# Kernel optimization log

Hardware: AMD Instinct MI355X
Metric: run time of the kernel (lower is better)

The kernel has to match this reference:

```python
import jax, jax.numpy as jnp
import numpy as np

N_NODES = 100000
N_EDGES = 1600000
N_FEAT = 128
HIDDEN = 128
N_CLASSES = 8
N_GRAPHS = 256


def setup_inputs() -> dict:
    key = jax.random.key(0)
    ks = jax.random.split(key, 10)
    x = jax.random.normal(ks[0], (N_NODES, N_FEAT), dtype=jnp.float32)
    edge_index = jax.random.randint(ks[1], (2, N_EDGES), 0, N_NODES, dtype=jnp.int64)
    batch = jnp.sort(jax.random.randint(ks[2], (N_NODES,), 0, N_GRAPHS, dtype=jnp.int64))
    s = 1.0 / np.sqrt(HIDDEN)
    W1 = jax.random.normal(ks[3], (N_FEAT, HIDDEN), dtype=jnp.float32) * s
    b1 = jnp.zeros((HIDDEN,), dtype=jnp.float32)
    W2 = jax.random.normal(ks[4], (HIDDEN, HIDDEN), dtype=jnp.float32) * s
    b2 = jnp.zeros((HIDDEN,), dtype=jnp.float32)
    W3 = jax.random.normal(ks[5], (HIDDEN, HIDDEN), dtype=jnp.float32) * s
    b3 = jnp.zeros((HIDDEN,), dtype=jnp.float32)
    Wc1 = jax.random.normal(ks[6], (HIDDEN, HIDDEN // 2), dtype=jnp.float32) * s
    bc1 = jnp.zeros((HIDDEN // 2,), dtype=jnp.float32)
    Wc2 = jax.random.normal(ks[7], (HIDDEN // 2, N_CLASSES), dtype=jnp.float32) * (1.0 / np.sqrt(HIDDEN // 2))
    bc2 = jnp.zeros((N_CLASSES,), dtype=jnp.float32)
    return dict(x=x, edge_index=edge_index, batch=batch, W1=W1, b1=b1,
                W2=W2, b2=b2, W3=W3, b3=b3, Wc1=Wc1, bc1=bc1, Wc2=Wc2, bc2=bc2)


def _gcn_conv(x, W, b, src, dst, dinv_src_dst, deg_inv):
    # PyG GCNConv: h = X W; out = sum_{j->i} norm_ij * h_j + deg_i^{-1} * h_i + b
    h = x @ W  # [N, H]
    msg = h[src] * dinv_src_dst[:, None]            # gather + scale  [E, H]
    agg = jax.ops.segment_sum(msg, dst, num_segments=N_NODES)
    agg = agg + h * deg_inv[:, None]                # self-loop term
    return agg + b


def reference(x, edge_index, batch, W1, b1, W2, b2, W3, b3, Wc1, bc1, Wc2, bc2):
    src, dst = edge_index[0], edge_index[1]
    # symmetric normalization with self-loops: deg_i = 1 + in-degree
    ones = jnp.ones((N_EDGES,), dtype=x.dtype)
    deg = jax.ops.segment_sum(ones, dst, num_segments=N_NODES) + 1.0
    dinv = jax.lax.rsqrt(deg)                        # deg^{-1/2}
    dinv_src_dst = dinv[src] * dinv[dst]             # norm per edge
    deg_inv = 1.0 / deg                              # self-loop norm

    h = jax.nn.relu(_gcn_conv(x, W1, b1, src, dst, dinv_src_dst, deg_inv))
    h = jax.nn.relu(_gcn_conv(h, W2, b2, src, dst, dinv_src_dst, deg_inv))
    h = jax.nn.relu(_gcn_conv(h, W3, b3, src, dst, dinv_src_dst, deg_inv))

    # global_mean_pool over batch ids
    sums = jax.ops.segment_sum(h, batch, num_segments=N_GRAPHS)
    counts = jax.ops.segment_sum(jnp.ones((N_NODES,), dtype=h.dtype), batch,
                                 num_segments=N_GRAPHS)
    pooled = sums / jnp.maximum(counts, 1.0)[:, None]  # [G, H]

    # classifier MLP (eval mode: dropout = identity)
    z = jax.nn.relu(pooled @ Wc1 + bc1)
    return z @ Wc2 + bc2
```

## Files before the change

### kernel.cpp

```cpp
#include <hip/hip_runtime.h>
#include <hip/hip_bf16.h>

#define N_NODES 100000
#define N_EDGES 1600000
#define NFEAT   128
#define HID     128
#define NG      256
#define NCLS    8

typedef __attribute__((ext_vector_type(8))) short bf16x8;
typedef __attribute__((ext_vector_type(4))) float f32x4;

__device__ __forceinline__ unsigned short f2bf(float f) {
    unsigned u = __float_as_uint(f);
    unsigned r = (u + 0x7fffu + ((u >> 16) & 1u)) >> 16;
    return (unsigned short)r;
}


__global__ void zero_int_kernel(int* __restrict__ p, int n) {
    int i = blockIdx.x * 256 + threadIdx.x;
    if (i < n) p[i] = 0;
}

__global__ void count_deg_kernel(const int* __restrict__ dst, int* __restrict__ deg, int e) {
    int i = blockIdx.x * 256 + threadIdx.x;
    if (i < e) atomicAdd(&deg[dst[i]], 1);
}

__global__ void scan1_kernel(const int* __restrict__ deg, int* __restrict__ tmp,
                             int* __restrict__ bsums, int n) {
    __shared__ int s[256];
    int t = threadIdx.x;
    int i = blockIdx.x * 256 + t;
    int v = (i < n) ? deg[i] : 0;
    s[t] = v;
    __syncthreads();
    for (int o = 1; o < 256; o <<= 1) {
        int a = (t >= o) ? s[t - o] : 0;
        __syncthreads();
        s[t] += a;
        __syncthreads();
    }
    if (i < n) tmp[i] = s[t];
    if (t == 255) bsums[blockIdx.x] = s[t];
}

__global__ void scan2_kernel(int* __restrict__ bsums, int nb) {
    __shared__ int s[512];
    int t = threadIdx.x;
    int v = (t < nb) ? bsums[t] : 0;
    s[t] = v;
    __syncthreads();
    for (int o = 1; o < 512; o <<= 1) {
        int a = (t >= o) ? s[t - o] : 0;
        __syncthreads();
        s[t] += a;
        __syncthreads();
    }
    if (t < nb) bsums[t] = s[t] - v;
}

__global__ void scan3_kernel(const int* __restrict__ tmp, const int* __restrict__ bsums,
                             const int* __restrict__ deg, int* __restrict__ row_ptr,
                             int* __restrict__ cursor, float* __restrict__ dinv,
                             float* __restrict__ deg_inv, int n) {
    int b = blockIdx.x;
    int i = b * 256 + threadIdx.x;
    if (i < n) {
        int g  = tmp[i] + bsums[b];
        int d  = deg[i];
        int rp = g - d;
        row_ptr[i] = rp;
        cursor[i]  = rp;
        float df = (float)d + 1.0f;
        dinv[i]    = rsqrtf(df);
        deg_inv[i] = 1.0f / df;
        if (i == n - 1) row_ptr[n] = g;
    }
}

__global__ void fill_edges_kernel(const int* __restrict__ src, const int* __restrict__ dst,
                                  const float* __restrict__ dinv, int* __restrict__ cursor,
                                  uint2* __restrict__ ed, int e) {
    int i = blockIdx.x * 256 + threadIdx.x;
    if (i < e) {
        int s = src[i], d = dst[i];
        int pos = atomicAdd(&cursor[d], 1);
        ed[pos] = make_uint2((unsigned)s, __float_as_uint(dinv[s] * dinv[d]));
    }
}

__global__ void cast_w_kernel(const float* __restrict__ W1, const float* __restrict__ W2,
                              const float* __restrict__ W3,
                              unsigned short* __restrict__ T1, unsigned short* __restrict__ T2,
                              unsigned short* __restrict__ T3) {
    int b = blockIdx.x;
    const float*    W = (b < 64) ? W1 : ((b < 128) ? W2 : W3);
    unsigned short* T = (b < 64) ? T1 : ((b < 128) ? T2 : T3);
    int i = (b & 63) * 256 + threadIdx.x;
    int k = i >> 7, n = i & 127;
    T[n * 128 + k] = f2bf(W[i]);
}

__global__ __launch_bounds__(256) void gemm_mfma_kernel(
        const float* __restrict__ in, unsigned short* __restrict__ H,
        const unsigned short* __restrict__ Wt) {
    const int tid  = threadIdx.x;
    const int wave = tid >> 6;
    const int lane = tid & 63;
    const int r16  = lane & 15;
    const int g    = lane >> 4;
    const int arow = blockIdx.x * 64 + wave * 16 + r16;
    const int arowc = (arow < N_NODES) ? arow : (N_NODES - 1);

    bf16x8 a[4];
#pragma unroll
    for (int kk = 0; kk < 4; ++kk) {
        const float* p = &in[(size_t)arowc * 128 + kk * 32 + g * 8];
        float4 lo = *(const float4*)p;
        float4 hi = *(const float4*)(p + 4);
        union { bf16x8 v; unsigned short u[8]; } t;
        t.u[0] = f2bf(lo.x); t.u[1] = f2bf(lo.y); t.u[2] = f2bf(lo.z); t.u[3] = f2bf(lo.w);
        t.u[4] = f2bf(hi.x); t.u[5] = f2bf(hi.y); t.u[6] = f2bf(hi.z); t.u[7] = f2bf(hi.w);
        a[kk] = t.v;
    }

    const bf16x8* Wv = (const bf16x8*)Wt;
    const int orow0 = blockIdx.x * 64 + wave * 16 + g * 4;

#pragma unroll
    for (int ct = 0; ct < 8; ++ct) {
        const int nb = (ct * 16 + r16) * 16 + g;
        f32x4 acc = {0.f, 0.f, 0.f, 0.f};
#pragma unroll
        for (int kk = 0; kk < 4; ++kk)
            acc = __builtin_amdgcn_mfma_f32_16x16x32_bf16(a[kk], Wv[nb + kk * 4], acc, 0, 0, 0);
        const int col = ct * 16 + r16;
#pragma unroll
        for (int i = 0; i < 4; ++i) {
            int gr = orow0 + i;
            if (gr < N_NODES) H[(size_t)gr * 128 + col] = f2bf(acc[i]);
        }
    }
}

__global__ __launch_bounds__(256) void spmm_bias_relu_kernel(
        const unsigned int* __restrict__ H,
        float* __restrict__ out,
        const int* __restrict__ row_ptr, const uint2* __restrict__ ed,
        const float* __restrict__ deg_inv, const float* __restrict__ bias) {
    int wave = threadIdx.x >> 6;
    int node = blockIdx.x * 4 + wave;
    int lane = threadIdx.x & 63;
    if (node >= N_NODES) return;

    float di = deg_inv[node];
    unsigned sv = H[(size_t)node * 64 + lane];
    float2 acc;
    acc.x = di * __uint_as_float(sv << 16);
    acc.y = di * __uint_as_float(sv & 0xffff0000u);

    int e  = row_ptr[node];
    int e1 = row_ptr[node + 1];
    for (; e + 1 < e1; e += 2) {
        uint2 d0 = ed[e], d1 = ed[e + 1];
        float w0 = __uint_as_float(d0.y);
        float w1 = __uint_as_float(d1.y);
        unsigned v0 = H[(size_t)d0.x * 64 + lane];
        unsigned v1 = H[(size_t)d1.x * 64 + lane];
        acc.x += w0 * __uint_as_float(v0 << 16);
        acc.y += w0 * __uint_as_float(v0 & 0xffff0000u);
        acc.x += w1 * __uint_as_float(v1 << 16);
        acc.y += w1 * __uint_as_float(v1 & 0xffff0000u);
    }
    if (e < e1) {
        uint2 d0 = ed[e];
        float w0 = __uint_as_float(d0.y);
        unsigned v0 = H[(size_t)d0.x * 64 + lane];
        acc.x += w0 * __uint_as_float(v0 << 16);
        acc.y += w0 * __uint_as_float(v0 & 0xffff0000u);
    }

    float2 b2 = ((const float2*)bias)[lane];
    float2 o;
    o.x = fmaxf(acc.x + b2.x, 0.f);
    o.y = fmaxf(acc.y + b2.y, 0.f);
    ((float2*)out)[(size_t)node * 64 + lane] = o;
}

__global__ __launch_bounds__(512) void pool_kernel(const float* __restrict__ H,
                                                   const int* __restrict__ batch,
                                                   float* __restrict__ pooled) {
    __shared__ float red[4][128];
    int g = blockIdx.x;
    int t = threadIdx.x;
    int f = t & 127;
    int s = t >> 7;

    int lo = 0, hi = N_NODES;
    while (lo < hi) { int mid = (lo + hi) >> 1; if (batch[mid] < g) lo = mid + 1; else hi = mid; }
    int start = lo;
    lo = start; hi = N_NODES;
    while (lo < hi) { int mid = (lo + hi) >> 1; if (batch[mid] < g + 1) lo = mid + 1; else hi = mid; }
    int end = lo;

    float acc = 0.f;
    for (int n = start + s; n < end; n += 4) acc += H[(size_t)n * 128 + f];
    red[s][f] = acc;
    __syncthreads();
    if (s == 0) {
        float v   = (red[0][f] + red[1][f]) + (red[2][f] + red[3][f]);
        float cnt = (float)(end - start);
        pooled[g * 128 + f] = v / fmaxf(cnt, 1.0f);
    }
}

__global__ void classify_kernel(const float* __restrict__ pooled,
                                const float* __restrict__ Wc1, const float* __restrict__ bc1,
                                const float* __restrict__ Wc2, const float* __restrict__ bc2,
                                float* __restrict__ out) {
    __shared__ float p[128];
    __shared__ float z[64];
    int g = blockIdx.x;
    int t = threadIdx.x;
    p[t]      = pooled[g * 128 + t];
    p[t + 64] = pooled[g * 128 + t + 64];
    __syncthreads();
    float a = bc1[t];
#pragma unroll 4
    for (int k = 0; k < 128; ++k) a += p[k] * Wc1[k * 64 + t];
    z[t] = fmaxf(a, 0.f);
    __syncthreads();
    if (t < 8) {
        float o = bc2[t];
#pragma unroll 8
        for (int j = 0; j < 64; ++j) o += z[j] * Wc2[j * 8 + t];
        out[g * 8 + t] = o;
    }
}


extern "C" void kernel_launch(void* const* d_in, const int* in_sizes, int n_in,
                              void* d_out, int out_size, void* d_ws, size_t ws_size,
                              hipStream_t stream) {
    const float* x    = (const float*)d_in[0];
    const int*   ei   = (const int*)d_in[1];
    const int*   bat  = (const int*)d_in[2];
    const float* W1   = (const float*)d_in[3];
    const float* b1   = (const float*)d_in[4];
    const float* W2   = (const float*)d_in[5];
    const float* b2   = (const float*)d_in[6];
    const float* W3   = (const float*)d_in[7];
    const float* b3   = (const float*)d_in[8];
    const float* Wc1  = (const float*)d_in[9];
    const float* bc1  = (const float*)d_in[10];
    const float* Wc2  = (const float*)d_in[11];
    const float* bc2  = (const float*)d_in[12];
    float* out = (float*)d_out;

    const int* src = ei;
    const int* dst = ei + N_EDGES;

    char* base = (char*)d_ws;
    size_t off = 0;
    auto alloc = [&](size_t bytes) -> void* {
        void* p = base + off;
        off = (off + bytes + 255) & ~(size_t)255;
        return p;
    };
    int*            deg_int = (int*)           alloc((size_t)N_NODES * 4);
    int*            tmp     = (int*)           alloc((size_t)N_NODES * 4);
    int*            bsums   = (int*)           alloc(512 * 4);
    int*            row_ptr = (int*)           alloc(((size_t)N_NODES + 1) * 4);
    int*            cursor  = (int*)           alloc((size_t)N_NODES * 4);
    float*          dinv    = (float*)         alloc((size_t)N_NODES * 4);
    float*          deg_inv = (float*)         alloc((size_t)N_NODES * 4);
    uint2*          edata   = (uint2*)         alloc((size_t)N_EDGES * 8);
    float*          bufA    = (float*)         alloc((size_t)N_NODES * 128 * 4);
    unsigned short* bufH    = (unsigned short*)alloc((size_t)N_NODES * 128 * 2);
    float*          pooled  = (float*)         alloc((size_t)NG * 128 * 4);
    unsigned short* Wt1     = (unsigned short*)alloc((size_t)HID * HID * 2);
    unsigned short* Wt2     = (unsigned short*)alloc((size_t)HID * HID * 2);
    unsigned short* Wt3     = (unsigned short*)alloc((size_t)HID * HID * 2);
    (void)ws_size; (void)n_in; (void)in_sizes; (void)out_size;

    const int nTilesN  = (N_NODES + 255) / 256;
    const int nBlocksE = (N_EDGES + 255) / 256;

    hipLaunchKernelGGL(cast_w_kernel, dim3(192), dim3(256), 0, stream, W1, W2, W3, Wt1, Wt2, Wt3);
    hipLaunchKernelGGL(zero_int_kernel, dim3(nTilesN), dim3(256), 0, stream, deg_int, N_NODES);
    hipLaunchKernelGGL(count_deg_kernel, dim3(nBlocksE), dim3(256), 0, stream, dst, deg_int, N_EDGES);
    hipLaunchKernelGGL(scan1_kernel, dim3(nTilesN), dim3(256), 0, stream, deg_int, tmp, bsums, N_NODES);
    hipLaunchKernelGGL(scan2_kernel, dim3(1), dim3(512), 0, stream, bsums, nTilesN);
    hipLaunchKernelGGL(scan3_kernel, dim3(nTilesN), dim3(256), 0, stream, tmp, bsums, deg_int,
                       row_ptr, cursor, dinv, deg_inv, N_NODES);
    hipLaunchKernelGGL(fill_edges_kernel, dim3(nBlocksE), dim3(256), 0, stream, src, dst, dinv,
                       cursor, edata, N_EDGES);

    const int gemmGrid = (N_NODES + 63) / 64;
    const int spmmGrid = N_NODES / 4;

    hipLaunchKernelGGL(gemm_mfma_kernel, dim3(gemmGrid), dim3(256), 0, stream, x, bufH, Wt1);
    hipLaunchKernelGGL(spmm_bias_relu_kernel, dim3(spmmGrid), dim3(256), 0, stream,
                       (const unsigned int*)bufH, bufA, row_ptr, edata, deg_inv, b1);
    hipLaunchKernelGGL(gemm_mfma_kernel, dim3(gemmGrid), dim3(256), 0, stream, bufA, bufH, Wt2);
    hipLaunchKernelGGL(spmm_bias_relu_kernel, dim3(spmmGrid), dim3(256), 0, stream,
                       (const unsigned int*)bufH, bufA, row_ptr, edata, deg_inv, b2);
    hipLaunchKernelGGL(gemm_mfma_kernel, dim3(gemmGrid), dim3(256), 0, stream, bufA, bufH, Wt3);
    hipLaunchKernelGGL(spmm_bias_relu_kernel, dim3(spmmGrid), dim3(256), 0, stream,
                       (const unsigned int*)bufH, bufA, row_ptr, edata, deg_inv, b3);

    hipLaunchKernelGGL(pool_kernel, dim3(NG), dim3(512), 0, stream, bufA, bat, pooled);
    hipLaunchKernelGGL(classify_kernel, dim3(NG), dim3(64), 0, stream, pooled, Wc1, bc1, Wc2, bc2, out);
}
```

Before: 731.4 us.

## Factor symmetric normalization into GEMM epilogue and drop per-edge weights

Prescales each GEMM output row by dinv and applies dinv of the destination after aggregation. The edge list then only needs column indices (4 bytes instead of 8 per edge), and the SpMM inner loop becomes plain adds. Also makes the edge-build kernels process four edges per thread and widens the pool kernel to 1024 threads. The extra bf16 rounding of the prescaled values slightly changes numerics.

```diff
diff --git a/kernel.cpp b/kernel.cpp
--- a/kernel.cpp
+++ b/kernel.cpp
@@ -23,9 +23,12 @@
     if (i < n) p[i] = 0;
 }
 
-__global__ void count_deg_kernel(const int* __restrict__ dst, int* __restrict__ deg, int e) {
-    int i = blockIdx.x * 256 + threadIdx.x;
-    if (i < e) atomicAdd(&deg[dst[i]], 1);
+__global__ void count_deg_kernel(const int* __restrict__ dst, int* __restrict__ deg) {
+    int t = blockIdx.x * 256 + threadIdx.x;
+    if (t >= N_EDGES / 4) return;
+#pragma unroll
+    for (int k = 0; k < 4; ++k)
+        atomicAdd(&deg[dst[t + k * (N_EDGES / 4)]], 1);
 }
 
 __global__ void scan1_kernel(const int* __restrict__ deg, int* __restrict__ tmp,
@@ -63,8 +66,7 @@
 
 __global__ void scan3_kernel(const int* __restrict__ tmp, const int* __restrict__ bsums,
                              const int* __restrict__ deg, int* __restrict__ row_ptr,
-                             int* __restrict__ cursor, float* __restrict__ dinv,
-                             float* __restrict__ deg_inv, int n) {
+                             int* __restrict__ cursor, float* __restrict__ dinv, int n) {
     int b = blockIdx.x;
     int i = b * 256 + threadIdx.x;
     if (i < n) {
@@ -73,21 +75,21 @@
         int rp = g - d;
         row_ptr[i] = rp;
         cursor[i]  = rp;
-        float df = (float)d + 1.0f;
-        dinv[i]    = rsqrtf(df);
-        deg_inv[i] = 1.0f / df;
+        dinv[i]    = rsqrtf((float)d + 1.0f);
         if (i == n - 1) row_ptr[n] = g;
     }
 }
 
 __global__ void fill_edges_kernel(const int* __restrict__ src, const int* __restrict__ dst,
-                                  const float* __restrict__ dinv, int* __restrict__ cursor,
-                                  uint2* __restrict__ ed, int e) {
-    int i = blockIdx.x * 256 + threadIdx.x;
-    if (i < e) {
+                                  int* __restrict__ cursor, int* __restrict__ col) {
+    int t = blockIdx.x * 256 + threadIdx.x;
+    if (t >= N_EDGES / 4) return;
+#pragma unroll
+    for (int k = 0; k < 4; ++k) {
+        int i = t + k * (N_EDGES / 4);
         int s = src[i], d = dst[i];
         int pos = atomicAdd(&cursor[d], 1);
-        ed[pos] = make_uint2((unsigned)s, __float_as_uint(dinv[s] * dinv[d]));
+        col[pos] = s;
     }
 }
 
@@ -104,8 +106,8 @@
 }
 
 __global__ __launch_bounds__(256) void gemm_mfma_kernel(
-        const float* __restrict__ in, unsigned short* __restrict__ H,
-        const unsigned short* __restrict__ Wt) {
+        const float* __restrict__ in, unsigned short* __restrict__ G,
+        const unsigned short* __restrict__ Wt, const float* __restrict__ dinv) {
     const int tid  = threadIdx.x;
     const int wave = tid >> 6;
     const int lane = tid & 63;
@@ -129,6 +131,13 @@
     const bf16x8* Wv = (const bf16x8*)Wt;
     const int orow0 = blockIdx.x * 64 + wave * 16 + g * 4;
 
+    float dv[4];
+#pragma unroll
+    for (int i = 0; i < 4; ++i) {
+        int gr = orow0 + i;
+        dv[i] = (gr < N_NODES) ? dinv[gr] : 0.f;
+    }
+
 #pragma unroll
     for (int ct = 0; ct < 8; ++ct) {
         const int nb = (ct * 16 + r16) * 16 + g;
@@ -140,59 +149,55 @@
 #pragma unroll
         for (int i = 0; i < 4; ++i) {
             int gr = orow0 + i;
-            if (gr < N_NODES) H[(size_t)gr * 128 + col] = f2bf(acc[i]);
+            if (gr < N_NODES) G[(size_t)gr * 128 + col] = f2bf(acc[i] * dv[i]);
         }
     }
 }
 
 __global__ __launch_bounds__(256) void spmm_bias_relu_kernel(
-        const unsigned int* __restrict__ H,
+        const unsigned int* __restrict__ G,
         float* __restrict__ out,
-        const int* __restrict__ row_ptr, const uint2* __restrict__ ed,
-        const float* __restrict__ deg_inv, const float* __restrict__ bias) {
+        const int* __restrict__ row_ptr, const int* __restrict__ col,
+        const float* __restrict__ dinv, const float* __restrict__ bias) {
     int wave = threadIdx.x >> 6;
     int node = blockIdx.x * 4 + wave;
     int lane = threadIdx.x & 63;
     if (node >= N_NODES) return;
 
-    float di = deg_inv[node];
-    unsigned sv = H[(size_t)node * 64 + lane];
+    unsigned sv = G[(size_t)node * 64 + lane];
     float2 acc;
-    acc.x = di * __uint_as_float(sv << 16);
-    acc.y = di * __uint_as_float(sv & 0xffff0000u);
+    acc.x = __uint_as_float(sv << 16);
+    acc.y = __uint_as_float(sv & 0xffff0000u);
 
     int e  = row_ptr[node];
     int e1 = row_ptr[node + 1];
     for (; e + 1 < e1; e += 2) {
-        uint2 d0 = ed[e], d1 = ed[e + 1];
-        float w0 = __uint_as_float(d0.y);
-        float w1 = __uint_as_float(d1.y);
-        unsigned v0 = H[(size_t)d0.x * 64 + lane];
-        unsigned v1 = H[(size_t)d1.x * 64 + lane];
-        acc.x += w0 * __uint_as_float(v0 << 16);
-        acc.y += w0 * __uint_as_float(v0 & 0xffff0000u);
-        acc.x += w1 * __uint_as_float(v1 << 16);
-        acc.y += w1 * __uint_as_float(v1 & 0xffff0000u);
+        int c0 = col[e], c1 = col[e + 1];
+        unsigned v0 = G[(size_t)c0 * 64 + lane];
+        unsigned v1 = G[(size_t)c1 * 64 + lane];
+        acc.x += __uint_as_float(v0 << 16);
+        acc.y += __uint_as_float(v0 & 0xffff0000u);
+        acc.x += __uint_as_float(v1 << 16);
+        acc.y += __uint_as_float(v1 & 0xffff0000u);
     }
     if (e < e1) {
-        uint2 d0 = ed[e];
-        float w0 = __uint_as_float(d0.y);
-        unsigned v0 = H[(size_t)d0.x * 64 + lane];
-        acc.x += w0 * __uint_as_float(v0 << 16);
-        acc.y += w0 * __uint_as_float(v0 & 0xffff0000u);
-    }
-
+        unsigned v0 = G[(size_t)col[e] * 64 + lane];
+        acc.x += __uint_as_float(v0 << 16);
+        acc.y += __uint_as_float(v0 & 0xffff0000u);
+    }
+
+    float di = dinv[node];
     float2 b2 = ((const float2*)bias)[lane];
     float2 o;
-    o.x = fmaxf(acc.x + b2.x, 0.f);
-    o.y = fmaxf(acc.y + b2.y, 0.f);
+    o.x = fmaxf(di * acc.x + b2.x, 0.f);
+    o.y = fmaxf(di * acc.y + b2.y, 0.f);
     ((float2*)out)[(size_t)node * 64 + lane] = o;
 }
 
-__global__ __launch_bounds__(512) void pool_kernel(const float* __restrict__ H,
-                                                   const int* __restrict__ batch,
-                                                   float* __restrict__ pooled) {
-    __shared__ float red[4][128];
+__global__ __launch_bounds__(1024) void pool_kernel(const float* __restrict__ H,
+                                                    const int* __restrict__ batch,
+                                                    float* __restrict__ pooled) {
+    __shared__ float red[8][128];
     int g = blockIdx.x;
     int t = threadIdx.x;
     int f = t & 127;
@@ -206,11 +211,12 @@
     int end = lo;
 
     float acc = 0.f;
-    for (int n = start + s; n < end; n += 4) acc += H[(size_t)n * 128 + f];
+    for (int n = start + s; n < end; n += 8) acc += H[(size_t)n * 128 + f];
     red[s][f] = acc;
     __syncthreads();
     if (s == 0) {
-        float v   = (red[0][f] + red[1][f]) + (red[2][f] + red[3][f]);
+        float v = ((red[0][f] + red[1][f]) + (red[2][f] + red[3][f]))
+                + ((red[4][f] + red[5][f]) + (red[6][f] + red[7][f]));
         float cnt = (float)(end - start);
         pooled[g * 128 + f] = v / fmaxf(cnt, 1.0f);
     }
@@ -275,42 +281,41 @@
     int*            row_ptr = (int*)           alloc(((size_t)N_NODES + 1) * 4);
     int*            cursor  = (int*)           alloc((size_t)N_NODES * 4);
     float*          dinv    = (float*)         alloc((size_t)N_NODES * 4);
-    float*          deg_inv = (float*)         alloc((size_t)N_NODES * 4);
-    uint2*          edata   = (uint2*)         alloc((size_t)N_EDGES * 8);
+    int*            colA    = (int*)           alloc((size_t)N_EDGES * 4);
     float*          bufA    = (float*)         alloc((size_t)N_NODES * 128 * 4);
-    unsigned short* bufH    = (unsigned short*)alloc((size_t)N_NODES * 128 * 2);
+    unsigned short* bufG    = (unsigned short*)alloc((size_t)N_NODES * 128 * 2);
     float*          pooled  = (float*)         alloc((size_t)NG * 128 * 4);
     unsigned short* Wt1     = (unsigned short*)alloc((size_t)HID * HID * 2);
     unsigned short* Wt2     = (unsigned short*)alloc((size_t)HID * HID * 2);
     unsigned short* Wt3     = (unsigned short*)alloc((size_t)HID * HID * 2);
     (void)ws_size; (void)n_in; (void)in_sizes; (void)out_size;
 
-    const int nTilesN  = (N_NODES + 255) / 256;
-    const int nBlocksE = (N_EDGES + 255) / 256;
+    const int nTilesN   = (N_NODES + 255) / 256;
+    const int nBlocksE4 = (N_EDGES / 4 + 255) / 256;
 
     hipLaunchKernelGGL(cast_w_kernel, dim3(192), dim3(256), 0, stream, W1, W2, W3, Wt1, Wt2, Wt3);
     hipLaunchKernelGGL(zero_int_kernel, dim3(nTilesN), dim3(256), 0, stream, deg_int, N_NODES);
-    hipLaunchKernelGGL(count_deg_kernel, dim3(nBlocksE), dim3(256), 0, stream, dst, deg_int, N_EDGES);
+    hipLaunchKernelGGL(count_deg_kernel, dim3(nBlocksE4), dim3(256), 0, stream, dst, deg_int);
     hipLaunchKernelGGL(scan1_kernel, dim3(nTilesN), dim3(256), 0, stream, deg_int, tmp, bsums, N_NODES);
     hipLaunchKernelGGL(scan2_kernel, dim3(1), dim3(512), 0, stream, bsums, nTilesN);
     hipLaunchKernelGGL(scan3_kernel, dim3(nTilesN), dim3(256), 0, stream, tmp, bsums, deg_int,
-                       row_ptr, cursor, dinv, deg_inv, N_NODES);
-    hipLaunchKernelGGL(fill_edges_kernel, dim3(nBlocksE), dim3(256), 0, stream, src, dst, dinv,
-                       cursor, edata, N_EDGES);
+                       row_ptr, cursor, dinv, N_NODES);
+    hipLaunchKernelGGL(fill_edges_kernel, dim3(nBlocksE4), dim3(256), 0, stream, src, dst,
+                       cursor, colA);
 
     const int gemmGrid = (N_NODES + 63) / 64;
     const int spmmGrid = N_NODES / 4;
 
-    hipLaunchKernelGGL(gemm_mfma_kernel, dim3(gemmGrid), dim3(256), 0, stream, x, bufH, Wt1);
+    hipLaunchKernelGGL(gemm_mfma_kernel, dim3(gemmGrid), dim3(256), 0, stream, x, bufG, Wt1, dinv);
     hipLaunchKernelGGL(spmm_bias_relu_kernel, dim3(spmmGrid), dim3(256), 0, stream,
-                       (const unsigned int*)bufH, bufA, row_ptr, edata, deg_inv, b1);
-    hipLaunchKernelGGL(gemm_mfma_kernel, dim3(gemmGrid), dim3(256), 0, stream, bufA, bufH, Wt2);
+                       (const unsigned int*)bufG, bufA, row_ptr, colA, dinv, b1);
+    hipLaunchKernelGGL(gemm_mfma_kernel, dim3(gemmGrid), dim3(256), 0, stream, bufA, bufG, Wt2, dinv);
     hipLaunchKernelGGL(spmm_bias_relu_kernel, dim3(spmmGrid), dim3(256), 0, stream,
-                       (const unsigned int*)bufH, bufA, row_ptr, edata, deg_inv, b2);
-    hipLaunchKernelGGL(gemm_mfma_kernel, dim3(gemmGrid), dim3(256), 0, stream, bufA, bufH, Wt3);
+                       (const unsigned int*)bufG, bufA, row_ptr, colA, dinv, b2);
+    hipLaunchKernelGGL(gemm_mfma_kernel, dim3(gemmGrid), dim3(256), 0, stream, bufA, bufG, Wt3, dinv);
     hipLaunchKernelGGL(spmm_bias_relu_kernel, dim3(spmmGrid), dim3(256), 0, stream,
-                       (const unsigned int*)bufH, bufA, row_ptr, edata, deg_inv, b3);
-
-    hipLaunchKernelGGL(pool_kernel, dim3(NG), dim3(512), 0, stream, bufA, bat, pooled);
+                       (const unsigned int*)bufG, bufA, row_ptr, colA, dinv, b3);
+
+    hipLaunchKernelGGL(pool_kernel, dim3(NG), dim3(1024), 0, stream, bufA, bat, pooled);
     hipLaunchKernelGGL(classify_kernel, dim3(NG), dim3(64), 0, stream, pooled, Wc1, bc1, Wc2, bc2, out);
 }
```

Measured after the change: 754.0 us. 3.1% more time.
